# Performance work log

Measured on AMD Instinct MI355X. Metric: run time of the kernel, lower is better.

## Reference

```python
import jax, jax.numpy as jnp
import numpy as np

N_NODES = 50000


def _sage_layer(x, edges, W_neigh, W_self, b):
    """HeteroGraphConv(sum) of per-relation DGL SAGEConv(mean).

    x:        [N, F_in] node features (single node type)
    edges:    [R, 2, E] int (src, dst) per relation
    W_neigh:  [R, F_in, F_out], W_self: [R, F_in, F_out], b: [R, F_out]
    returns:  [N, F_out]
    """
    N = x.shape[0]
    R = edges.shape[0]
    out = jnp.zeros((N, W_neigh.shape[-1]), dtype=x.dtype)
    for r in range(R):  # small fixed number of relation types
        src = edges[r, 0]
        dst = edges[r, 1]
        # mean-aggregate neighbor features onto dst
        s = jax.ops.segment_sum(x[src], dst, num_segments=N)          # [N, F_in]
        deg = jax.ops.segment_sum(jnp.ones_like(dst, dtype=x.dtype), dst,
                                  num_segments=N)                     # [N]
        mean = s / jnp.maximum(deg, 1.0)[:, None]                     # zero-deg -> 0
        # SAGEConv(mean): fc_self(h_dst) + fc_neigh(mean_neigh) + bias
        out = out + x @ W_self[r] + mean @ W_neigh[r] + b[r]
    return out


def setup_inputs() -> dict:
    key = jax.random.key(0)
    ks = jax.random.split(key, 10)
    F_in, H, O, R, E = 128, 128, 64, 2, 800000
    scale_in = 1.0 / np.sqrt(F_in)
    scale_h = 1.0 / np.sqrt(H)
    return {
        "x": jax.random.normal(ks[0], (N_NODES, F_in), dtype=jnp.float32),
        "edges": jax.random.randint(ks[1], (R, 2, E), 0, N_NODES, dtype=jnp.int32),
        "neg_edges": jax.random.randint(ks[2], (2, E), 0, N_NODES, dtype=jnp.int32),
        "W_neigh1": jax.random.normal(ks[3], (R, F_in, H), jnp.float32) * scale_in,
        "W_self1": jax.random.normal(ks[4], (R, F_in, H), jnp.float32) * scale_in,
        "b1": jnp.zeros((R, H), jnp.float32),
        "W_neigh2": jax.random.normal(ks[5], (R, H, O), jnp.float32) * scale_h,
        "W_self2": jax.random.normal(ks[6], (R, H, O), jnp.float32) * scale_h,
        "b2": jnp.zeros((R, O), jnp.float32),
    }


def reference(x, edges, neg_edges, W_neigh1, W_self1, b1, W_neigh2, W_self2, b2):
    h = _sage_layer(x, edges, W_neigh1, W_self1, b1)
    h = jax.nn.relu(h)
    h = _sage_layer(h, edges, W_neigh2, W_self2, b2)          # [N, O]
    # HeteroDotProductPredictor: u_dot_v on edges of the scored etype (rel 0)
    pos_score = jnp.sum(h[edges[0, 0]] * h[edges[0, 1]], axis=-1)      # [E]
    neg_score = jnp.sum(h[neg_edges[0]] * h[neg_edges[1]], axis=-1)    # [E_neg]
    return pos_score, neg_score
```

## Files before the change

### kernel.cpp

```cpp
#include <hip/hip_runtime.h>


#define BW 128
#define NBK_MAX 1024
#define EPB 8192

typedef __attribute__((ext_vector_type(8))) short bf16x8;
typedef __attribute__((ext_vector_type(4))) float floatx4;
typedef __attribute__((ext_vector_type(2))) float floatx2;

__device__ __forceinline__ unsigned short f2bf(float f) {
    unsigned u = __float_as_uint(f);
    unsigned r = u + 0x7FFFu + ((u >> 16) & 1u);
    return (unsigned short)(r >> 16);
}
__device__ __forceinline__ unsigned pack2(float a, float b) {
    return (unsigned)f2bf(a) | ((unsigned)f2bf(b) << 16);
}
__device__ __forceinline__ float bflo(unsigned v) { return __uint_as_float(v << 16); }
__device__ __forceinline__ float bfhi(unsigned v) { return __uint_as_float(v & 0xFFFF0000u); }
#define RFL(x) __builtin_amdgcn_readfirstlane(x)

#if defined(__has_builtin) && __has_builtin(__builtin_amdgcn_cvt_pk_f32_fp8)
__device__ __forceinline__ floatx2 fp8lo(unsigned v) {
    return __builtin_amdgcn_cvt_pk_f32_fp8((int)v, false);
}
__device__ __forceinline__ floatx2 fp8hi(unsigned v) {
    return __builtin_amdgcn_cvt_pk_f32_fp8((int)v, true);
}
#else
__device__ __forceinline__ float fp8_1(unsigned b) {
    return __uint_as_float(((b & 0x80u) << 24) | ((b & 0x7Fu) << 20)) * 0x1.0p+120f;
}
__device__ __forceinline__ floatx2 fp8lo(unsigned v) {
    floatx2 r; r.x = fp8_1(v & 0xFFu); r.y = fp8_1((v >> 8) & 0xFFu); return r;
}
__device__ __forceinline__ floatx2 fp8hi(unsigned v) {
    floatx2 r; r.x = fp8_1((v >> 16) & 0xFFu); r.y = fp8_1((v >> 24) & 0xFFu); return r;
}
#endif

#if defined(__has_builtin) && __has_builtin(__builtin_amdgcn_cvt_pk_fp8_f32)
__device__ __forceinline__ unsigned f32x4_fp8x4(float a, float b, float c, float d) {
    unsigned lo = __builtin_amdgcn_cvt_pk_fp8_f32(a, b, 0, false);
    return __builtin_amdgcn_cvt_pk_fp8_f32(c, d, lo, true);
}
__device__ __forceinline__ unsigned char f2fp8_1(float x) {
    return (unsigned char)(__builtin_amdgcn_cvt_pk_fp8_f32(x, x, 0, false) & 0xFFu);
}
#else
__device__ __forceinline__ unsigned f2fp8(float x) {
    float m = fminf(fabsf(x), 448.0f);
    unsigned u = __float_as_uint(m * 0x1.0p-120f);
    unsigned r = (u + 0x7FFFFu + ((u >> 20) & 1u)) >> 20;
    if (r > 0x7Eu) r = 0x7Eu;
    return r | ((__float_as_uint(x) >> 24) & 0x80u);
}
__device__ __forceinline__ unsigned f32x4_fp8x4(float a, float b, float c, float d) {
    return f2fp8(a) | (f2fp8(b) << 8) | (f2fp8(c) << 16) | (f2fp8(d) << 24);
}
__device__ __forceinline__ unsigned char f2fp8_1(float x) {
    return (unsigned char)f2fp8(x);
}
#endif

__global__ __launch_bounds__(256) void
bucket_count_kernel(const int* __restrict__ edges, int* __restrict__ bcnt,
                    int NBK, int E)
{
    __shared__ int cnt[2 * NBK_MAX];
    const int rbT = 2 * NBK;
    const int t = threadIdx.x;
    for (int k = t; k < rbT; k += 256) cnt[k] = 0;
    __syncthreads();
    long long start = (long long)blockIdx.x * EPB;
    long long twoE = 2LL * E;
    for (int u = 0; u < EPB / 256; ++u) {
        long long idx = start + u * 256 + t;
        if (idx < twoE) {
            int r = idx >= E;
            int e = (int)(idx - (long long)r * E);
            int d = edges[(size_t)r * 2 * E + E + e];
            atomicAdd(&cnt[r * NBK + (d >> 7)], 1);
        }
    }
    __syncthreads();
    for (int k = t; k < rbT; k += 256)
        if (cnt[k]) atomicAdd(&bcnt[k], cnt[k]);
}

__global__ __launch_bounds__(1024) void
bucket_scan_kernel(const int* __restrict__ bcnt, int* __restrict__ bko,
                   int rbT, int twoE)
{
    __shared__ int sm[1024];
    int t = threadIdx.x;
    int v = (t < rbT) ? bcnt[t] : 0;
    sm[t] = v;
    __syncthreads();
    for (int s = 1; s < 1024; s <<= 1) {
        int u = (t >= s) ? sm[t - s] : 0;
        __syncthreads();
        sm[t] += u;
        __syncthreads();
    }
    if (t < rbT) bko[t] = sm[t] - v;
    if (t == 0) bko[rbT] = twoE;
}

__global__ __launch_bounds__(256) void
partition_kernel(const int* __restrict__ edges, const int* __restrict__ bko,
                 int* __restrict__ gcur, uint2* __restrict__ staging,
                 int NBK, int E)
{
    __shared__ int cnt[2 * NBK_MAX];
    __shared__ int base[2 * NBK_MAX];
    const int rbT = 2 * NBK;
    const int t = threadIdx.x;
    for (int k = t; k < rbT; k += 256) cnt[k] = 0;
    __syncthreads();
    long long start = (long long)blockIdx.x * EPB;
    long long twoE = 2LL * E;
    for (int u = 0; u < EPB / 256; ++u) {
        long long idx = start + u * 256 + t;
        if (idx < twoE) {
            int r = idx >= E;
            int e = (int)(idx - (long long)r * E);
            int d = edges[(size_t)r * 2 * E + E + e];
            atomicAdd(&cnt[r * NBK + (d >> 7)], 1);
        }
    }
    __syncthreads();
    for (int k = t; k < rbT; k += 256) {
        int c0 = cnt[k];
        if (c0) base[k] = bko[k] + atomicAdd(&gcur[k], c0);
        cnt[k] = 0;
    }
    __syncthreads();
    for (int u = 0; u < EPB / 256; ++u) {
        long long idx = start + u * 256 + t;
        if (idx < twoE) {
            int r = idx >= E;
            int e = (int)(idx - (long long)r * E);
            int s = edges[(size_t)r * 2 * E + e];
            int d = edges[(size_t)r * 2 * E + E + e];
            int rb = r * NBK + (d >> 7);
            int pos = atomicAdd(&cnt[rb], 1);
            staging[(size_t)base[rb] + pos] = make_uint2((unsigned)s, (unsigned)d);
        }
    }
}

__global__ __launch_bounds__(256) void
bucket_csr_kernel(const uint2* __restrict__ staging, const int* __restrict__ bko,
                  int* __restrict__ csr, int* __restrict__ off,
                  int NBK, int N)
{
    __shared__ int hist[BW], excl[BW], cur[BW], sc[BW];
    const int rb = blockIdx.x;
    const int r = rb / NBK;
    const int b = rb % NBK;
    const int node0 = b * BW;
    const int nn = min(BW, N - node0);
    const int cbase = bko[rb];
    const int c = bko[rb + 1] - cbase;
    const int t = threadIdx.x;

    if (t < BW) { hist[t] = 0; cur[t] = 0; }
    __syncthreads();
    for (int k = t; k < c; k += 256)
        atomicAdd(&hist[(int)staging[(size_t)cbase + k].y - node0], 1);
    __syncthreads();
    if (t < BW) sc[t] = hist[t];
    __syncthreads();
    for (int s = 1; s < BW; s <<= 1) {
        int v = (t < BW && t >= s) ? sc[t - s] : 0;
        __syncthreads();
        if (t < BW) sc[t] += v;
        __syncthreads();
    }
    if (t < BW) excl[t] = sc[t] - hist[t];
    if (t < nn) off[(size_t)r * N + node0 + t] = cbase + excl[t];
    __syncthreads();
    for (int k = t; k < c; k += 256) {
        uint2 pr = staging[(size_t)cbase + k];
        int l = (int)pr.y - node0;
        int pos = atomicAdd(&cur[l], 1);
        csr[(size_t)cbase + excl[l] + pos] = (int)pr.x;
    }
}

__global__ void cvt_kernel(const float* __restrict__ in,
                           unsigned short* __restrict__ o,
                           unsigned char* __restrict__ o8, int n4)
{
    int t = blockIdx.x * blockDim.x + threadIdx.x;
    if (t >= n4) return;
    float4 v = ((const float4*)in)[t];
    ushort4 r;
    r.x = f2bf(v.x); r.y = f2bf(v.y); r.z = f2bf(v.z); r.w = f2bf(v.w);
    ((ushort4*)o)[t] = r;
    ((unsigned*)o8)[t] = f32x4_fp8x4(v.x, v.y, v.z, v.w);
}

__global__ void prep_kernel(const float* __restrict__ Ws1, const float* __restrict__ Wn1,
                            const float* __restrict__ b1,
                            const float* __restrict__ Ws2, const float* __restrict__ Wn2,
                            const float* __restrict__ b2,
                            unsigned short* __restrict__ WT1z, unsigned short* __restrict__ WT1a,
                            unsigned short* __restrict__ WT1b, float* __restrict__ bc1,
                            unsigned short* __restrict__ WT2z, unsigned short* __restrict__ WT2a,
                            unsigned short* __restrict__ WT2b, float* __restrict__ bc2)
{
    int t = blockIdx.x * blockDim.x + threadIdx.x;
    if (t < 16384) {
        int n = t >> 7, k = t & 127;
        int in = k * 128 + n;
        WT1z[t] = f2bf(Ws1[in] + Ws1[16384 + in]);
        WT1a[t] = f2bf(Wn1[in]);
        WT1b[t] = f2bf(Wn1[16384 + in]);
    }
    if (t < 8192) {
        int n = t >> 7, k = t & 127;
        int in = k * 64 + n;
        WT2z[t] = f2bf(Ws2[in] + Ws2[8192 + in]);
        WT2a[t] = f2bf(Wn2[in]);
        WT2b[t] = f2bf(Wn2[8192 + in]);
    }
    if (t < 128) bc1[t] = b1[t] + b1[128 + t];
    if (t < 64)  bc2[t] = b2[t] + b2[64 + t];
}

__global__ __launch_bounds__(256) void
agg1_kernel(const unsigned char* __restrict__ xb8,
            const int* __restrict__ csr, const int* __restrict__ off,
            unsigned short* __restrict__ m0, unsigned short* __restrict__ m1,
            int N, int twoE)
{
    int w = blockIdx.x * 4 + (threadIdx.x >> 6);
    int lane = threadIdx.x & 63;
    if (w >= N) return;
    const int col = lane * 2;
    const unsigned char* xc = xb8 + col;

    float sx0 = 0.f, sy0 = 0.f, sx1 = 0.f, sy1 = 0.f;

    int o0 = RFL(off[w]);
    int o1 = RFL(off[w + 1]);
    int d0 = o1 - o0;
    int j = o0;
    for (; j + 7 < o1; j += 8) {
        int s0 = RFL(csr[j]);     int s1 = RFL(csr[j + 1]);
        int s2 = RFL(csr[j + 2]); int s3 = RFL(csr[j + 3]);
        int s4 = RFL(csr[j + 4]); int s5 = RFL(csr[j + 5]);
        int s6 = RFL(csr[j + 6]); int s7 = RFL(csr[j + 7]);
        unsigned a0 = *(const unsigned short*)(xc + (size_t)s0 * 128);
        unsigned a1 = *(const unsigned short*)(xc + (size_t)s1 * 128);
        unsigned a2 = *(const unsigned short*)(xc + (size_t)s2 * 128);
        unsigned a3 = *(const unsigned short*)(xc + (size_t)s3 * 128);
        unsigned a4 = *(const unsigned short*)(xc + (size_t)s4 * 128);
        unsigned a5 = *(const unsigned short*)(xc + (size_t)s5 * 128);
        unsigned a6 = *(const unsigned short*)(xc + (size_t)s6 * 128);
        unsigned a7 = *(const unsigned short*)(xc + (size_t)s7 * 128);
        floatx2 v0 = fp8lo(a0); floatx2 v1 = fp8lo(a1);
        floatx2 v2 = fp8lo(a2); floatx2 v3 = fp8lo(a3);
        floatx2 v4 = fp8lo(a4); floatx2 v5 = fp8lo(a5);
        floatx2 v6 = fp8lo(a6); floatx2 v7 = fp8lo(a7);
        sx0 += ((v0.x + v1.x) + (v2.x + v3.x)) + ((v4.x + v5.x) + (v6.x + v7.x));
        sy0 += ((v0.y + v1.y) + (v2.y + v3.y)) + ((v4.y + v5.y) + (v6.y + v7.y));
    }
    for (; j < o1; ++j) {
        int s0 = RFL(csr[j]);
        floatx2 v = fp8lo(*(const unsigned short*)(xc + (size_t)s0 * 128));
        sx0 += v.x; sy0 += v.y;
    }

    int p = N + w;
    o0 = RFL(off[p]);
    o1 = (p + 1 < 2 * N) ? RFL(off[p + 1]) : twoE;
    int d1 = o1 - o0;
    j = o0;
    for (; j + 7 < o1; j += 8) {
        int s0 = RFL(csr[j]);     int s1 = RFL(csr[j + 1]);
        int s2 = RFL(csr[j + 2]); int s3 = RFL(csr[j + 3]);
        int s4 = RFL(csr[j + 4]); int s5 = RFL(csr[j + 5]);
        int s6 = RFL(csr[j + 6]); int s7 = RFL(csr[j + 7]);
        unsigned a0 = *(const unsigned short*)(xc + (size_t)s0 * 128);
        unsigned a1 = *(const unsigned short*)(xc + (size_t)s1 * 128);
        unsigned a2 = *(const unsigned short*)(xc + (size_t)s2 * 128);
        unsigned a3 = *(const unsigned short*)(xc + (size_t)s3 * 128);
        unsigned a4 = *(const unsigned short*)(xc + (size_t)s4 * 128);
        unsigned a5 = *(const unsigned short*)(xc + (size_t)s5 * 128);
        unsigned a6 = *(const unsigned short*)(xc + (size_t)s6 * 128);
        unsigned a7 = *(const unsigned short*)(xc + (size_t)s7 * 128);
        floatx2 v0 = fp8lo(a0); floatx2 v1 = fp8lo(a1);
        floatx2 v2 = fp8lo(a2); floatx2 v3 = fp8lo(a3);
        floatx2 v4 = fp8lo(a4); floatx2 v5 = fp8lo(a5);
        floatx2 v6 = fp8lo(a6); floatx2 v7 = fp8lo(a7);
        sx1 += ((v0.x + v1.x) + (v2.x + v3.x)) + ((v4.x + v5.x) + (v6.x + v7.x));
        sy1 += ((v0.y + v1.y) + (v2.y + v3.y)) + ((v4.y + v5.y) + (v6.y + v7.y));
    }
    for (; j < o1; ++j) {
        int s0 = RFL(csr[j]);
        floatx2 v = fp8lo(*(const unsigned short*)(xc + (size_t)s0 * 128));
        sx1 += v.x; sy1 += v.y;
    }

    float inv0 = 1.0f / fmaxf((float)d0, 1.0f);
    float inv1 = 1.0f / fmaxf((float)d1, 1.0f);
    *(unsigned*)(m0 + (size_t)w * 128 + col) = pack2(sx0 * inv0, sy0 * inv0);
    *(unsigned*)(m1 + (size_t)w * 128 + col) = pack2(sx1 * inv1, sy1 * inv1);
}

__global__ __launch_bounds__(256) void
gemm1_fused_kernel(const unsigned short* __restrict__ xb,
                   const unsigned short* __restrict__ m0,
                   const unsigned short* __restrict__ m1,
                   const unsigned short* __restrict__ WTz,
                   const unsigned short* __restrict__ WTa,
                   const unsigned short* __restrict__ WTb,
                   const float* __restrict__ bias,
                   unsigned short* __restrict__ h1b, int N)
{
    const int tid = threadIdx.x;
    const int wave = tid >> 6;
    const int lane = tid & 63;
    const int m = lane & 15;
    const int quad = lane >> 4;
    const int colbase = blockIdx.y * 64;

    floatx4 acc[4];
    const floatx4 z4 = {0.f, 0.f, 0.f, 0.f};
#pragma unroll
    for (int t = 0; t < 4; ++t) acc[t] = z4;

    int arow = blockIdx.x * 64 + wave * 16 + m;
    if (arow >= N) arow = N - 1;
    const size_t ab = (size_t)arow * 128 + quad * 8;

    bf16x8 ax0 = *(const bf16x8*)(xb + ab);
    bf16x8 ax1 = *(const bf16x8*)(xb + ab + 32);
    bf16x8 ax2 = *(const bf16x8*)(xb + ab + 64);
    bf16x8 ax3 = *(const bf16x8*)(xb + ab + 96);
    bf16x8 a00 = *(const bf16x8*)(m0 + ab);
    bf16x8 a01 = *(const bf16x8*)(m0 + ab + 32);
    bf16x8 a02 = *(const bf16x8*)(m0 + ab + 64);
    bf16x8 a03 = *(const bf16x8*)(m0 + ab + 96);
    bf16x8 a10 = *(const bf16x8*)(m1 + ab);
    bf16x8 a11 = *(const bf16x8*)(m1 + ab + 32);
    bf16x8 a12 = *(const bf16x8*)(m1 + ab + 64);
    bf16x8 a13 = *(const bf16x8*)(m1 + ab + 96);

#pragma unroll
    for (int t = 0; t < 4; ++t) {
        const size_t bo = (size_t)(colbase + t * 16 + m) * 128 + quad * 8;
        acc[t] = __builtin_amdgcn_mfma_f32_16x16x32_bf16(
            ax0, *(const bf16x8*)(WTz + bo), acc[t], 0, 0, 0);
        acc[t] = __builtin_amdgcn_mfma_f32_16x16x32_bf16(
            a00, *(const bf16x8*)(WTa + bo), acc[t], 0, 0, 0);
        acc[t] = __builtin_amdgcn_mfma_f32_16x16x32_bf16(
            a10, *(const bf16x8*)(WTb + bo), acc[t], 0, 0, 0);
        acc[t] = __builtin_amdgcn_mfma_f32_16x16x32_bf16(
            ax1, *(const bf16x8*)(WTz + bo + 32), acc[t], 0, 0, 0);
        acc[t] = __builtin_amdgcn_mfma_f32_16x16x32_bf16(
            a01, *(const bf16x8*)(WTa + bo + 32), acc[t], 0, 0, 0);
        acc[t] = __builtin_amdgcn_mfma_f32_16x16x32_bf16(
            a11, *(const bf16x8*)(WTb + bo + 32), acc[t], 0, 0, 0);
        acc[t] = __builtin_amdgcn_mfma_f32_16x16x32_bf16(
            ax2, *(const bf16x8*)(WTz + bo + 64), acc[t], 0, 0, 0);
        acc[t] = __builtin_amdgcn_mfma_f32_16x16x32_bf16(
            a02, *(const bf16x8*)(WTa + bo + 64), acc[t], 0, 0, 0);
        acc[t] = __builtin_amdgcn_mfma_f32_16x16x32_bf16(
            a12, *(const bf16x8*)(WTb + bo + 64), acc[t], 0, 0, 0);
        acc[t] = __builtin_amdgcn_mfma_f32_16x16x32_bf16(
            ax3, *(const bf16x8*)(WTz + bo + 96), acc[t], 0, 0, 0);
        acc[t] = __builtin_amdgcn_mfma_f32_16x16x32_bf16(
            a03, *(const bf16x8*)(WTa + bo + 96), acc[t], 0, 0, 0);
        acc[t] = __builtin_amdgcn_mfma_f32_16x16x32_bf16(
            a13, *(const bf16x8*)(WTb + bo + 96), acc[t], 0, 0, 0);
    }

    const int gr0 = blockIdx.x * 64 + wave * 16 + quad * 4;
#pragma unroll
    for (int t = 0; t < 4; ++t) {
        int colg = colbase + t * 16 + m;
        float bv = bias[colg];
#pragma unroll
        for (int i = 0; i < 4; ++i) {
            int gr = gr0 + i;
            if (gr < N)
                h1b[(size_t)gr * 128 + colg] = f2bf(fmaxf(acc[t][i] + bv, 0.0f));
        }
    }
}

__global__ __launch_bounds__(256) void
gemm2_fused_kernel(const unsigned short* __restrict__ Ab,
                   const unsigned short* __restrict__ WTz,
                   const unsigned short* __restrict__ WTa,
                   const unsigned short* __restrict__ WTb,
                   const float* __restrict__ bias,
                   float* __restrict__ zf,
                   unsigned char* __restrict__ t08, unsigned char* __restrict__ t18,
                   int N)
{
    const int tid = threadIdx.x;
    const int wave = tid >> 6;
    const int lane = tid & 63;
    const int m = lane & 15;
    const int quad = lane >> 4;

    floatx4 accz[4], acca[4], accb[4];
    const floatx4 z4 = {0.f, 0.f, 0.f, 0.f};
#pragma unroll
    for (int t = 0; t < 4; ++t) { accz[t] = z4; acca[t] = z4; accb[t] = z4; }

    int arow = blockIdx.x * 64 + wave * 16 + m;
    if (arow >= N) arow = N - 1;
    const size_t ab = (size_t)arow * 128 + quad * 8;

    bf16x8 h0 = *(const bf16x8*)(Ab + ab);
    bf16x8 h1 = *(const bf16x8*)(Ab + ab + 32);
    bf16x8 h2 = *(const bf16x8*)(Ab + ab + 64);
    bf16x8 h3 = *(const bf16x8*)(Ab + ab + 96);

#pragma unroll
    for (int t = 0; t < 4; ++t) {
        const size_t bo = (size_t)(t * 16 + m) * 128 + quad * 8;
        accz[t] = __builtin_amdgcn_mfma_f32_16x16x32_bf16(
            h0, *(const bf16x8*)(WTz + bo), accz[t], 0, 0, 0);
        acca[t] = __builtin_amdgcn_mfma_f32_16x16x32_bf16(
            h0, *(const bf16x8*)(WTa + bo), acca[t], 0, 0, 0);
        accb[t] = __builtin_amdgcn_mfma_f32_16x16x32_bf16(
            h0, *(const bf16x8*)(WTb + bo), accb[t], 0, 0, 0);
        accz[t] = __builtin_amdgcn_mfma_f32_16x16x32_bf16(
            h1, *(const bf16x8*)(WTz + bo + 32), accz[t], 0, 0, 0);
        acca[t] = __builtin_amdgcn_mfma_f32_16x16x32_bf16(
            h1, *(const bf16x8*)(WTa + bo + 32), acca[t], 0, 0, 0);
        accb[t] = __builtin_amdgcn_mfma_f32_16x16x32_bf16(
            h1, *(const bf16x8*)(WTb + bo + 32), accb[t], 0, 0, 0);
        accz[t] = __builtin_amdgcn_mfma_f32_16x16x32_bf16(
            h2, *(const bf16x8*)(WTz + bo + 64), accz[t], 0, 0, 0);
        acca[t] = __builtin_amdgcn_mfma_f32_16x16x32_bf16(
            h2, *(const bf16x8*)(WTa + bo + 64), acca[t], 0, 0, 0);
        accb[t] = __builtin_amdgcn_mfma_f32_16x16x32_bf16(
            h2, *(const bf16x8*)(WTb + bo + 64), accb[t], 0, 0, 0);
        accz[t] = __builtin_amdgcn_mfma_f32_16x16x32_bf16(
            h3, *(const bf16x8*)(WTz + bo + 96), accz[t], 0, 0, 0);
        acca[t] = __builtin_amdgcn_mfma_f32_16x16x32_bf16(
            h3, *(const bf16x8*)(WTa + bo + 96), acca[t], 0, 0, 0);
        accb[t] = __builtin_amdgcn_mfma_f32_16x16x32_bf16(
            h3, *(const bf16x8*)(WTb + bo + 96), accb[t], 0, 0, 0);
    }

    const int gr0 = blockIdx.x * 64 + wave * 16 + quad * 4;
#pragma unroll
    for (int t = 0; t < 4; ++t) {
        int colg = t * 16 + m;
        float bv = bias[colg];
#pragma unroll
        for (int i = 0; i < 4; ++i) {
            int gr = gr0 + i;
            if (gr < N) {
                zf[(size_t)gr * 64 + colg] = accz[t][i] + bv;
                t08[(size_t)gr * 64 + colg] = f2fp8_1(acca[t][i]);
                t18[(size_t)gr * 64 + colg] = f2fp8_1(accb[t][i]);
            }
        }
    }
}

__global__ __launch_bounds__(256) void
agg2_kernel(const unsigned char* __restrict__ t08,
            const unsigned char* __restrict__ t18,
            const float* __restrict__ z2,
            const int* __restrict__ csr, const int* __restrict__ off,
            unsigned short* __restrict__ h2b, int N, int twoE)
{
    int w = blockIdx.x * 4 + (threadIdx.x >> 6);
    int lane = threadIdx.x & 63;
    if (w >= N) return;
    const int q = lane >> 4;
    const int col = (lane & 15) * 4;
    const unsigned char* t0c = t08 + col;
    const unsigned char* t1c = t18 + col;

    float a0 = 0.f, a1 = 0.f, a2 = 0.f, a3 = 0.f;
    float b0 = 0.f, b1 = 0.f, b2 = 0.f, b3 = 0.f;

    int o0 = RFL(off[w]);
    int o1 = RFL(off[w + 1]);
    int d0 = o1 - o0;
    int j = o0;
    for (; j + 15 < o1; j += 16) {
        int r0 = csr[j + q];
        int r1 = csr[j + 4 + q];
        int r2 = csr[j + 8 + q];
        int r3 = csr[j + 12 + q];
        unsigned v0 = *(const unsigned*)(t0c + (size_t)r0 * 64);
        unsigned v1 = *(const unsigned*)(t0c + (size_t)r1 * 64);
        unsigned v2 = *(const unsigned*)(t0c + (size_t)r2 * 64);
        unsigned v3 = *(const unsigned*)(t0c + (size_t)r3 * 64);
        floatx2 l0 = fp8lo(v0), h0 = fp8hi(v0);
        floatx2 l1 = fp8lo(v1), h1 = fp8hi(v1);
        floatx2 l2 = fp8lo(v2), h2 = fp8hi(v2);
        floatx2 l3 = fp8lo(v3), h3 = fp8hi(v3);
        a0 += (l0.x + l1.x) + (l2.x + l3.x);
        a1 += (l0.y + l1.y) + (l2.y + l3.y);
        a2 += (h0.x + h1.x) + (h2.x + h3.x);
        a3 += (h0.y + h1.y) + (h2.y + h3.y);
    }
    for (; j + 3 < o1; j += 4) {
        int r = csr[j + q];
        unsigned v = *(const unsigned*)(t0c + (size_t)r * 64);
        floatx2 l = fp8lo(v), h = fp8hi(v);
        a0 += l.x; a1 += l.y; a2 += h.x; a3 += h.y;
    }
    if (j < o1 && q < o1 - j) {
        int r = csr[j + q];
        unsigned v = *(const unsigned*)(t0c + (size_t)r * 64);
        floatx2 l = fp8lo(v), h = fp8hi(v);
        a0 += l.x; a1 += l.y; a2 += h.x; a3 += h.y;
    }

    int p = N + w;
    o0 = RFL(off[p]);
    o1 = (p + 1 < 2 * N) ? RFL(off[p + 1]) : twoE;
    int d1 = o1 - o0;
    j = o0;
    for (; j + 15 < o1; j += 16) {
        int r0 = csr[j + q];
        int r1 = csr[j + 4 + q];
        int r2 = csr[j + 8 + q];
        int r3 = csr[j + 12 + q];
        unsigned v0 = *(const unsigned*)(t1c + (size_t)r0 * 64);
        unsigned v1 = *(const unsigned*)(t1c + (size_t)r1 * 64);
        unsigned v2 = *(const unsigned*)(t1c + (size_t)r2 * 64);
        unsigned v3 = *(const unsigned*)(t1c + (size_t)r3 * 64);
        floatx2 l0 = fp8lo(v0), h0 = fp8hi(v0);
        floatx2 l1 = fp8lo(v1), h1 = fp8hi(v1);
        floatx2 l2 = fp8lo(v2), h2 = fp8hi(v2);
        floatx2 l3 = fp8lo(v3), h3 = fp8hi(v3);
        b0 += (l0.x + l1.x) + (l2.x + l3.x);
        b1 += (l0.y + l1.y) + (l2.y + l3.y);
        b2 += (h0.x + h1.x) + (h2.x + h3.x);
        b3 += (h0.y + h1.y) + (h2.y + h3.y);
    }
    for (; j + 3 < o1; j += 4) {
        int r = csr[j + q];
        unsigned v = *(const unsigned*)(t1c + (size_t)r * 64);
        floatx2 l = fp8lo(v), h = fp8hi(v);
        b0 += l.x; b1 += l.y; b2 += h.x; b3 += h.y;
    }
    if (j < o1 && q < o1 - j) {
        int r = csr[j + q];
        unsigned v = *(const unsigned*)(t1c + (size_t)r * 64);
        floatx2 l = fp8lo(v), h = fp8hi(v);
        b0 += l.x; b1 += l.y; b2 += h.x; b3 += h.y;
    }

    a0 += __shfl_xor(a0, 16); a1 += __shfl_xor(a1, 16);
    a2 += __shfl_xor(a2, 16); a3 += __shfl_xor(a3, 16);
    b0 += __shfl_xor(b0, 16); b1 += __shfl_xor(b1, 16);
    b2 += __shfl_xor(b2, 16); b3 += __shfl_xor(b3, 16);
    a0 += __shfl_xor(a0, 32); a1 += __shfl_xor(a1, 32);
    a2 += __shfl_xor(a2, 32); a3 += __shfl_xor(a3, 32);
    b0 += __shfl_xor(b0, 32); b1 += __shfl_xor(b1, 32);
    b2 += __shfl_xor(b2, 32); b3 += __shfl_xor(b3, 32);
    if (q == 0) {
        float inv0 = 1.0f / fmaxf((float)d0, 1.0f);
        float inv1 = 1.0f / fmaxf((float)d1, 1.0f);
        float4 z = *(const float4*)(z2 + (size_t)w * 64 + col);
        float h0v = z.x + a0 * inv0 + b0 * inv1;
        float h1v = z.y + a1 * inv0 + b1 * inv1;
        float h2v = z.z + a2 * inv0 + b2 * inv1;
        float h3v = z.w + a3 * inv0 + b3 * inv1;
        uint2 u;
        u.x = pack2(h0v, h1v);
        u.y = pack2(h2v, h3v);
        *(uint2*)(h2b + (size_t)w * 64 + col) = u;
    }
}

__global__ __launch_bounds__(256) void
score_kernel(const unsigned short* __restrict__ h,
             const int* __restrict__ edges, const int* __restrict__ neg,
             float* __restrict__ out, int E, int En)
{
    int t = blockIdx.x * blockDim.x + threadIdx.x;
    int e = t >> 3;
    int c = t & 7;
    if (e >= E + En) return;
    int sI, dI, oI;
    if (e < E) { sI = edges[e]; dI = edges[E + e]; oI = e; }
    else { int en = e - E; sI = neg[en]; dI = neg[En + en]; oI = E + en; }
    uint4 va = *(const uint4*)(h + (size_t)sI * 64 + c * 8);
    uint4 vb = *(const uint4*)(h + (size_t)dI * 64 + c * 8);
    float s = 0.0f;
    s = fmaf(bflo(va.x), bflo(vb.x), s);
    s = fmaf(bfhi(va.x), bfhi(vb.x), s);
    s = fmaf(bflo(va.y), bflo(vb.y), s);
    s = fmaf(bfhi(va.y), bfhi(vb.y), s);
    s = fmaf(bflo(va.z), bflo(vb.z), s);
    s = fmaf(bfhi(va.z), bfhi(vb.z), s);
    s = fmaf(bflo(va.w), bflo(vb.w), s);
    s = fmaf(bfhi(va.w), bfhi(vb.w), s);
    s += __shfl_xor(s, 1);
    s += __shfl_xor(s, 2);
    s += __shfl_xor(s, 4);
    if (c == 0) out[oI] = s;
}

extern "C" void kernel_launch(void* const* d_in, const int* in_sizes, int n_in,
                              void* d_out, int out_size, void* d_ws, size_t ws_size,
                              hipStream_t stream)
{
    const float* x     = (const float*)d_in[0];
    const int*   edges = (const int*)d_in[1];
    const int*   neg   = (const int*)d_in[2];
    const float* Wn1   = (const float*)d_in[3];
    const float* Ws1   = (const float*)d_in[4];
    const float* b1    = (const float*)d_in[5];
    const float* Wn2   = (const float*)d_in[6];
    const float* Ws2   = (const float*)d_in[7];
    const float* b2    = (const float*)d_in[8];
    float* out = (float*)d_out;

    const int Fin = 128, R = 2;
    const int N  = in_sizes[0] / Fin;
    const int E  = in_sizes[1] / (R * 2);
    const int En = in_sizes[2] / 2;
    const int twoE = 2 * E;
    const int NBK = (N + BW - 1) / BW;
    const int rbT = 2 * NBK;

    const size_t nb128 = (size_t)N * 128 * sizeof(unsigned short);
    char* p = (char*)d_ws;

    uint2* staging       = (uint2*)p;
    unsigned char* xb8   = (unsigned char*)p;
    float* z2            = (float*)p;
    {
        size_t r0 = (size_t)twoE * sizeof(uint2);
        size_t r1 = (size_t)N * 64 * sizeof(float);
        size_t r2 = (size_t)N * 128;
        size_t rm = r0 > r1 ? r0 : r1;
        if (r2 > rm) rm = r2;
        p += rm;
    }
    unsigned short* m0  = (unsigned short*)p; p += nb128;
    unsigned short* m1  = (unsigned short*)p; p += nb128;
    unsigned short* xb  = (unsigned short*)p; p += nb128;
    unsigned short* h1b = (unsigned short*)p; p += nb128;
    unsigned short* WT1z = (unsigned short*)p; p += 16384 * 2;
    unsigned short* WT1a = (unsigned short*)p; p += 16384 * 2;
    unsigned short* WT1b = (unsigned short*)p; p += 16384 * 2;
    unsigned short* WT2z = (unsigned short*)p; p += 8192 * 2;
    unsigned short* WT2a = (unsigned short*)p; p += 8192 * 2;
    unsigned short* WT2b = (unsigned short*)p; p += 8192 * 2;
    float* bc1 = (float*)p; p += 128 * sizeof(float);
    float* bc2 = (float*)p; p += 64 * sizeof(float);
    int* bcnt = (int*)p; p += (size_t)2 * NBK_MAX * sizeof(int);
    int* gcur = (int*)p; p += (size_t)2 * NBK_MAX * sizeof(int);
    int* bko  = (int*)p; p += ((size_t)2 * NBK_MAX + 1) * sizeof(int);
    int* off  = (int*)p; p += (size_t)2 * N * sizeof(int);
    int* csr  = (int*)p;

    unsigned char*  t08 = (unsigned char*)m0;
    unsigned char*  t18 = t08 + (size_t)N * 64;
    unsigned short* h2b = m1;

    const int BS = 256;
    const int edge_blocks = (twoE + EPB - 1) / EPB;
    const int gx = (N + 63) / 64;

    hipMemsetAsync(bcnt, 0, (size_t)4 * NBK_MAX * sizeof(int), stream);
    bucket_count_kernel<<<edge_blocks, BS, 0, stream>>>(edges, bcnt, NBK, E);
    bucket_scan_kernel<<<1, 1024, 0, stream>>>(bcnt, bko, rbT, twoE);
    partition_kernel<<<edge_blocks, BS, 0, stream>>>(edges, bko, gcur, staging, NBK, E);
    bucket_csr_kernel<<<rbT, BS, 0, stream>>>(staging, bko, csr, off, NBK, N);

    cvt_kernel<<<(N * 32 + BS - 1) / BS, BS, 0, stream>>>(x, xb, xb8, N * 32);
    prep_kernel<<<(16384 + BS - 1) / BS, BS, 0, stream>>>(
        Ws1, Wn1, b1, Ws2, Wn2, b2,
        WT1z, WT1a, WT1b, bc1, WT2z, WT2a, WT2b, bc2);

    agg1_kernel<<<(N + 3) / 4, BS, 0, stream>>>(xb8, csr, off, m0, m1, N, twoE);
    {
        dim3 g(gx, 2);
        gemm1_fused_kernel<<<g, BS, 0, stream>>>(xb, m0, m1, WT1z, WT1a, WT1b,
                                                 bc1, h1b, N);
    }

    gemm2_fused_kernel<<<gx, BS, 0, stream>>>(h1b, WT2z, WT2a, WT2b, bc2,
                                              z2, t08, t18, N);
    agg2_kernel<<<(N + 3) / 4, BS, 0, stream>>>(t08, t18, z2, csr, off, h2b, N, twoE);

    score_kernel<<<((E + En) * 8 + BS - 1) / BS, BS, 0, stream>>>(
        h2b, edges, neg, out, E, En);
}
```

Measured before the change: 363.6 us.

## Stage GEMM weight tiles in swizzled LDS and double rows per block

Both fused GEMM kernels now cooperatively load the three 64x128 bf16 weight tiles into shared memory once per block, using an XOR swizzle to avoid bank conflicts, and read MFMA B operands from LDS instead of global memory. Blocks grow to 512 threads covering 128 rows, so each staged tile is reused by eight waves. This is meant to cut redundant global and L2 traffic for weights. In exchange it adds a block-wide sync and 48KB of LDS per block, which may limit occupancy.

```diff
diff --git a/kernel.cpp b/kernel.cpp
--- a/kernel.cpp
+++ b/kernel.cpp
@@ -312,7 +312,14 @@
     *(unsigned*)(m1 + (size_t)w * 128 + col) = pack2(sx1 * inv1, sy1 * inv1);
 }
 
-__global__ __launch_bounds__(256) void
+__device__ __forceinline__ bf16x8 bs_read(const unsigned short* Bs, int mat,
+                                          int c, int s, int quad) {
+    unsigned byte = (unsigned)(mat * 16384 + c * 256 + s * 64 + quad * 16);
+    byte ^= (unsigned)((c & 7) << 4);
+    return *(const bf16x8*)((const char*)Bs + byte);
+}
+
+__global__ __launch_bounds__(512) void
 gemm1_fused_kernel(const unsigned short* __restrict__ xb,
                    const unsigned short* __restrict__ m0,
                    const unsigned short* __restrict__ m1,
@@ -322,6 +329,8 @@
                    const float* __restrict__ bias,
                    unsigned short* __restrict__ h1b, int N)
 {
+    __shared__ unsigned short Bs[3 * 64 * 128];
+
     const int tid = threadIdx.x;
     const int wave = tid >> 6;
     const int lane = tid & 63;
@@ -329,12 +338,26 @@
     const int quad = lane >> 4;
     const int colbase = blockIdx.y * 64;
 
+#pragma unroll
+    for (int i = 0; i < 6; ++i) {
+        int o = (i * 512 + tid) * 8;
+        int mat = o >> 13;
+        int rem = o & 8191;
+        int c = rem >> 7;
+        int k = rem & 127;
+        const unsigned short* src = (mat == 0) ? WTz : ((mat == 1) ? WTa : WTb);
+        uint4 v = *(const uint4*)(src + (size_t)(colbase + c) * 128 + k);
+        unsigned byte = (unsigned)(o * 2) ^ (unsigned)((c & 7) << 4);
+        *(uint4*)((char*)Bs + byte) = v;
+    }
+    __syncthreads();
+
     floatx4 acc[4];
     const floatx4 z4 = {0.f, 0.f, 0.f, 0.f};
 #pragma unroll
     for (int t = 0; t < 4; ++t) acc[t] = z4;
 
-    int arow = blockIdx.x * 64 + wave * 16 + m;
+    int arow = blockIdx.x * 128 + wave * 16 + m;
     if (arow >= N) arow = N - 1;
     const size_t ab = (size_t)arow * 128 + quad * 8;
 
@@ -353,34 +376,34 @@
 
 #pragma unroll
     for (int t = 0; t < 4; ++t) {
-        const size_t bo = (size_t)(colbase + t * 16 + m) * 128 + quad * 8;
-        acc[t] = __builtin_amdgcn_mfma_f32_16x16x32_bf16(
-            ax0, *(const bf16x8*)(WTz + bo), acc[t], 0, 0, 0);
-        acc[t] = __builtin_amdgcn_mfma_f32_16x16x32_bf16(
-            a00, *(const bf16x8*)(WTa + bo), acc[t], 0, 0, 0);
-        acc[t] = __builtin_amdgcn_mfma_f32_16x16x32_bf16(
-            a10, *(const bf16x8*)(WTb + bo), acc[t], 0, 0, 0);
-        acc[t] = __builtin_amdgcn_mfma_f32_16x16x32_bf16(
-            ax1, *(const bf16x8*)(WTz + bo + 32), acc[t], 0, 0, 0);
-        acc[t] = __builtin_amdgcn_mfma_f32_16x16x32_bf16(
-            a01, *(const bf16x8*)(WTa + bo + 32), acc[t], 0, 0, 0);
-        acc[t] = __builtin_amdgcn_mfma_f32_16x16x32_bf16(
-            a11, *(const bf16x8*)(WTb + bo + 32), acc[t], 0, 0, 0);
-        acc[t] = __builtin_amdgcn_mfma_f32_16x16x32_bf16(
-            ax2, *(const bf16x8*)(WTz + bo + 64), acc[t], 0, 0, 0);
-        acc[t] = __builtin_amdgcn_mfma_f32_16x16x32_bf16(
-            a02, *(const bf16x8*)(WTa + bo + 64), acc[t], 0, 0, 0);
-        acc[t] = __builtin_amdgcn_mfma_f32_16x16x32_bf16(
-            a12, *(const bf16x8*)(WTb + bo + 64), acc[t], 0, 0, 0);
-        acc[t] = __builtin_amdgcn_mfma_f32_16x16x32_bf16(
-            ax3, *(const bf16x8*)(WTz + bo + 96), acc[t], 0, 0, 0);
-        acc[t] = __builtin_amdgcn_mfma_f32_16x16x32_bf16(
-            a03, *(const bf16x8*)(WTa + bo + 96), acc[t], 0, 0, 0);
-        acc[t] = __builtin_amdgcn_mfma_f32_16x16x32_bf16(
-            a13, *(const bf16x8*)(WTb + bo + 96), acc[t], 0, 0, 0);
-    }
-
-    const int gr0 = blockIdx.x * 64 + wave * 16 + quad * 4;
+        const int c = t * 16 + m;
+        acc[t] = __builtin_amdgcn_mfma_f32_16x16x32_bf16(
+            ax0, bs_read(Bs, 0, c, 0, quad), acc[t], 0, 0, 0);
+        acc[t] = __builtin_amdgcn_mfma_f32_16x16x32_bf16(
+            a00, bs_read(Bs, 1, c, 0, quad), acc[t], 0, 0, 0);
+        acc[t] = __builtin_amdgcn_mfma_f32_16x16x32_bf16(
+            a10, bs_read(Bs, 2, c, 0, quad), acc[t], 0, 0, 0);
+        acc[t] = __builtin_amdgcn_mfma_f32_16x16x32_bf16(
+            ax1, bs_read(Bs, 0, c, 1, quad), acc[t], 0, 0, 0);
+        acc[t] = __builtin_amdgcn_mfma_f32_16x16x32_bf16(
+            a01, bs_read(Bs, 1, c, 1, quad), acc[t], 0, 0, 0);
+        acc[t] = __builtin_amdgcn_mfma_f32_16x16x32_bf16(
+            a11, bs_read(Bs, 2, c, 1, quad), acc[t], 0, 0, 0);
+        acc[t] = __builtin_amdgcn_mfma_f32_16x16x32_bf16(
+            ax2, bs_read(Bs, 0, c, 2, quad), acc[t], 0, 0, 0);
+        acc[t] = __builtin_amdgcn_mfma_f32_16x16x32_bf16(
+            a02, bs_read(Bs, 1, c, 2, quad), acc[t], 0, 0, 0);
+        acc[t] = __builtin_amdgcn_mfma_f32_16x16x32_bf16(
+            a12, bs_read(Bs, 2, c, 2, quad), acc[t], 0, 0, 0);
+        acc[t] = __builtin_amdgcn_mfma_f32_16x16x32_bf16(
+            ax3, bs_read(Bs, 0, c, 3, quad), acc[t], 0, 0, 0);
+        acc[t] = __builtin_amdgcn_mfma_f32_16x16x32_bf16(
+            a03, bs_read(Bs, 1, c, 3, quad), acc[t], 0, 0, 0);
+        acc[t] = __builtin_amdgcn_mfma_f32_16x16x32_bf16(
+            a13, bs_read(Bs, 2, c, 3, quad), acc[t], 0, 0, 0);
+    }
+
+    const int gr0 = blockIdx.x * 128 + wave * 16 + quad * 4;
 #pragma unroll
     for (int t = 0; t < 4; ++t) {
         int colg = colbase + t * 16 + m;
@@ -394,7 +417,7 @@
     }
 }
 
-__global__ __launch_bounds__(256) void
+__global__ __launch_bounds__(512) void
 gemm2_fused_kernel(const unsigned short* __restrict__ Ab,
                    const unsigned short* __restrict__ WTz,
                    const unsigned short* __restrict__ WTa,
@@ -404,18 +427,34 @@
                    unsigned char* __restrict__ t08, unsigned char* __restrict__ t18,
                    int N)
 {
+    __shared__ unsigned short Bs[3 * 64 * 128];
+
     const int tid = threadIdx.x;
     const int wave = tid >> 6;
     const int lane = tid & 63;
     const int m = lane & 15;
     const int quad = lane >> 4;
 
+#pragma unroll
+    for (int i = 0; i < 6; ++i) {
+        int o = (i * 512 + tid) * 8;
+        int mat = o >> 13;
+        int rem = o & 8191;
+        int c = rem >> 7;
+        int k = rem & 127;
+        const unsigned short* src = (mat == 0) ? WTz : ((mat == 1) ? WTa : WTb);
+        uint4 v = *(const uint4*)(src + (size_t)c * 128 + k);
+        unsigned byte = (unsigned)(o * 2) ^ (unsigned)((c & 7) << 4);
+        *(uint4*)((char*)Bs + byte) = v;
+    }
+    __syncthreads();
+
     floatx4 accz[4], acca[4], accb[4];
     const floatx4 z4 = {0.f, 0.f, 0.f, 0.f};
 #pragma unroll
     for (int t = 0; t < 4; ++t) { accz[t] = z4; acca[t] = z4; accb[t] = z4; }
 
-    int arow = blockIdx.x * 64 + wave * 16 + m;
+    int arow = blockIdx.x * 128 + wave * 16 + m;
     if (arow >= N) arow = N - 1;
     const size_t ab = (size_t)arow * 128 + quad * 8;
 
@@ -426,34 +465,34 @@
 
 #pragma unroll
     for (int t = 0; t < 4; ++t) {
-        const size_t bo = (size_t)(t * 16 + m) * 128 + quad * 8;
+        const int c = t * 16 + m;
         accz[t] = __builtin_amdgcn_mfma_f32_16x16x32_bf16(
-            h0, *(const bf16x8*)(WTz + bo), accz[t], 0, 0, 0);
+            h0, bs_read(Bs, 0, c, 0, quad), accz[t], 0, 0, 0);
         acca[t] = __builtin_amdgcn_mfma_f32_16x16x32_bf16(
-            h0, *(const bf16x8*)(WTa + bo), acca[t], 0, 0, 0);
+            h0, bs_read(Bs, 1, c, 0, quad), acca[t], 0, 0, 0);
         accb[t] = __builtin_amdgcn_mfma_f32_16x16x32_bf16(
-            h0, *(const bf16x8*)(WTb + bo), accb[t], 0, 0, 0);
+            h0, bs_read(Bs, 2, c, 0, quad), accb[t], 0, 0, 0);
         accz[t] = __builtin_amdgcn_mfma_f32_16x16x32_bf16(
-            h1, *(const bf16x8*)(WTz + bo + 32), accz[t], 0, 0, 0);
+            h1, bs_read(Bs, 0, c, 1, quad), accz[t], 0, 0, 0);
         acca[t] = __builtin_amdgcn_mfma_f32_16x16x32_bf16(
-            h1, *(const bf16x8*)(WTa + bo + 32), acca[t], 0, 0, 0);
+            h1, bs_read(Bs, 1, c, 1, quad), acca[t], 0, 0, 0);
         accb[t] = __builtin_amdgcn_mfma_f32_16x16x32_bf16(
-            h1, *(const bf16x8*)(WTb + bo + 32), accb[t], 0, 0, 0);
+            h1, bs_read(Bs, 2, c, 1, quad), accb[t], 0, 0, 0);
         accz[t] = __builtin_amdgcn_mfma_f32_16x16x32_bf16(
-            h2, *(const bf16x8*)(WTz + bo + 64), accz[t], 0, 0, 0);
+            h2, bs_read(Bs, 0, c, 2, quad), accz[t], 0, 0, 0);
         acca[t] = __builtin_amdgcn_mfma_f32_16x16x32_bf16(
-            h2, *(const bf16x8*)(WTa + bo + 64), acca[t], 0, 0, 0);
+            h2, bs_read(Bs, 1, c, 2, quad), acca[t], 0, 0, 0);
         accb[t] = __builtin_amdgcn_mfma_f32_16x16x32_bf16(
-            h2, *(const bf16x8*)(WTb + bo + 64), accb[t], 0, 0, 0);
+            h2, bs_read(Bs, 2, c, 2, quad), accb[t], 0, 0, 0);
         accz[t] = __builtin_amdgcn_mfma_f32_16x16x32_bf16(
-            h3, *(const bf16x8*)(WTz + bo + 96), accz[t], 0, 0, 0);
+            h3, bs_read(Bs, 0, c, 3, quad), accz[t], 0, 0, 0);
         acca[t] = __builtin_amdgcn_mfma_f32_16x16x32_bf16(
-            h3, *(const bf16x8*)(WTa + bo + 96), acca[t], 0, 0, 0);
+            h3, bs_read(Bs, 1, c, 3, quad), acca[t], 0, 0, 0);
         accb[t] = __builtin_amdgcn_mfma_f32_16x16x32_bf16(
-            h3, *(const bf16x8*)(WTb + bo + 96), accb[t], 0, 0, 0);
-    }
-
-    const int gr0 = blockIdx.x * 64 + wave * 16 + quad * 4;
+            h3, bs_read(Bs, 2, c, 3, quad), accb[t], 0, 0, 0);
+    }
+
+    const int gr0 = blockIdx.x * 128 + wave * 16 + quad * 4;
 #pragma unroll
     for (int t = 0; t < 4; ++t) {
         int colg = t * 16 + m;
@@ -672,7 +711,7 @@
 
     const int BS = 256;
     const int edge_blocks = (twoE + EPB - 1) / EPB;
-    const int gx = (N + 63) / 64;
+    const int gx128 = (N + 127) / 128;
 
     hipMemsetAsync(bcnt, 0, (size_t)4 * NBK_MAX * sizeof(int), stream);
     bucket_count_kernel<<<edge_blocks, BS, 0, stream>>>(edges, bcnt, NBK, E);
@@ -687,13 +726,13 @@
 
     agg1_kernel<<<(N + 3) / 4, BS, 0, stream>>>(xb8, csr, off, m0, m1, N, twoE);
     {
-        dim3 g(gx, 2);
-        gemm1_fused_kernel<<<g, BS, 0, stream>>>(xb, m0, m1, WT1z, WT1a, WT1b,
-                                                 bc1, h1b, N);
-    }
-
-    gemm2_fused_kernel<<<gx, BS, 0, stream>>>(h1b, WT2z, WT2a, WT2b, bc2,
-                                              z2, t08, t18, N);
+        dim3 g(gx128, 2);
+        gemm1_fused_kernel<<<g, 512, 0, stream>>>(xb, m0, m1, WT1z, WT1a, WT1b,
+                                                  bc1, h1b, N);
+    }
+
+    gemm2_fused_kernel<<<gx128, 512, 0, stream>>>(h1b, WT2z, WT2a, WT2b, bc2,
+                                                  z2, t08, t18, N);
     agg2_kernel<<<(N + 3) / 4, BS, 0, stream>>>(t08, t18, z2, csr, off, h2b, N, twoE);
 
     score_kernel<<<((E + En) * 8 + BS - 1) / BS, BS, 0, stream>>>(
```

Result: faster. 318.3 us (-12.5%).
